# Kernel tuning notes

Hardware: AMD Instinct MI355X
Metric: run time of the kernel (lower is better)

Reference implementation:

```python
import jax, jax.numpy as jnp
import numpy as np

B, N, D = 8, 1024, 512
H = 8
DH = D // H
EPS_DIST = 1e-8
EPS_LN = 1e-5


def _layer_norm(x, gamma, beta):
    mu = jnp.mean(x, axis=-1, keepdims=True)
    var = jnp.mean((x - mu) ** 2, axis=-1, keepdims=True)
    return (x - mu) * jax.lax.rsqrt(var + EPS_LN) * gamma + beta


def setup_inputs() -> dict:
    key = jax.random.key(0)
    ks = jax.random.split(key, 6)
    scale = 1.0 / np.sqrt(D)
    inp = {
        "x": jax.random.normal(ks[0], (B, N, D), dtype=jnp.float32),
        "Wq": jax.random.normal(ks[1], (D, D), dtype=jnp.float32) * scale,
        "Wk": jax.random.normal(ks[2], (D, D), dtype=jnp.float32) * scale,
        "Wv": jax.random.normal(ks[3], (D, D), dtype=jnp.float32) * scale,
        "Wo": jax.random.normal(ks[4], (D, D), dtype=jnp.float32) * scale,
        "bq": jnp.zeros((D,), jnp.float32),
        "bk": jnp.zeros((D,), jnp.float32),
        "bv": jnp.zeros((D,), jnp.float32),
        "bo": jnp.zeros((D,), jnp.float32),
        "ln1_g": jnp.ones((D,), jnp.float32),
        "ln1_b": jnp.zeros((D,), jnp.float32),
        "ln2_g": jnp.ones((D,), jnp.float32),
        "ln2_b": jnp.zeros((D,), jnp.float32),
    }
    return inp


def reference(x, Wq, bq, Wk, bk, Wv, bv, Wo, bo, ln1_g, ln1_b, ln2_g, ln2_b):
    residual = x
    h = _layer_norm(x, ln1_g, ln1_b)  # pre-norm

    def heads(t):
        # [B,N,D] -> [B,H,N,DH]
        return t.reshape(B, N, H, DH).transpose(0, 2, 1, 3)

    q = heads(h @ Wq + bq)
    k = heads(h @ Wk + bk)
    v = heads(h @ Wv + bv)

    # Euclidean pairwise distance via ||q||^2 + ||k||^2 - 2 q.k expansion
    q_sq = jnp.sum(q * q, axis=-1)[..., :, None]      # [B,H,N,1]
    k_sq = jnp.sum(k * k, axis=-1)[..., None, :]      # [B,H,1,N]
    qk = jnp.einsum("bhnd,bhmd->bhnm", q, k)          # [B,H,N,N]
    d2 = jnp.maximum(q_sq + k_sq - 2.0 * qk, 0.0)
    dist = jnp.sqrt(d2 + EPS_DIST)

    # distance -> attention score: smaller distance = higher attention
    attn = jax.nn.softmax(-dist, axis=-1)             # [B,H,N,N]

    out = jnp.einsum("bhnm,bhmd->bhnd", attn, v)      # [B,H,N,DH]
    out = out.transpose(0, 2, 1, 3).reshape(B, N, D)
    out = out @ Wo + bo

    y = residual + out
    y = _layer_norm(y, ln2_g, ln2_b)
    return y
```

## Files before the change

kernel.cpp:

```cpp
#include <hip/hip_runtime.h>
#include <math.h>

typedef __attribute__((ext_vector_type(8))) short short8;
typedef __attribute__((ext_vector_type(4))) float f32x4;

constexpr int B  = 8;
constexpr int N  = 1024;
constexpr int D  = 512;
constexpr int H  = 8;
constexpr int DH = 64;
constexpr int M_ROWS = 8192;
constexpr float EPS_DIST = 1e-8f;
constexpr float EPS_LN   = 1e-5f;

__device__ inline unsigned short bfbits(float f) {
    union { float f; unsigned u; } v; v.f = f;
    unsigned r = v.u + 0x7fffu + ((v.u >> 16) & 1u);
    return (unsigned short)(r >> 16);
}
__device__ inline float bf2f(unsigned short s) {
    union { unsigned u; float f; } v; v.u = ((unsigned)s) << 16; return v.f;
}

__device__ inline void async_ld16(unsigned short* lds, const unsigned short* g) {
    __builtin_amdgcn_global_load_lds(
        (const __attribute__((address_space(1))) unsigned int*)(g),
        (__attribute__((address_space(3))) unsigned int*)(lds),
        16, 0, 0);
}

__device__ inline float block_sum256(float s, float* red) {
    for (int o = 32; o > 0; o >>= 1) s += __shfl_down(s, o, 64);
    int lane = threadIdx.x & 63, wid = threadIdx.x >> 6;
    if (lane == 0) red[wid] = s;
    __syncthreads();
    if (threadIdx.x == 0) red[4] = red[0] + red[1] + red[2] + red[3];
    __syncthreads();
    return red[4];
}

__global__ __launch_bounds__(256) void prep_kernel(const float* __restrict__ Wq,
                                                   const float* __restrict__ Wk,
                                                   const float* __restrict__ Wv,
                                                   const float* __restrict__ Wo,
                                                   unsigned short* __restrict__ WtAll,
                                                   const float* __restrict__ x,
                                                   const float* __restrict__ ln1_g,
                                                   const float* __restrict__ ln1_b,
                                                   unsigned short* __restrict__ h_bf) {
    __shared__ float red[8];
    const int bxg = blockIdx.x;
    if (bxg < 256) {
        int sub = bxg >> 6;
        const float* W = sub == 0 ? Wq : sub == 1 ? Wk : sub == 2 ? Wv : Wo;
        unsigned short* Wt = WtAll + (size_t)sub * 262144;
        int t = (bxg & 63) * 256 + threadIdx.x;
        int tn = t & 127, tk = t >> 7;
        int k = tk * 4, n = tn * 4;
        float4 r0 = *(const float4*)&W[(size_t)(k + 0) * 512 + n];
        float4 r1 = *(const float4*)&W[(size_t)(k + 1) * 512 + n];
        float4 r2 = *(const float4*)&W[(size_t)(k + 2) * 512 + n];
        float4 r3 = *(const float4*)&W[(size_t)(k + 3) * 512 + n];
        ushort4 c;
        c.x = bfbits(r0.x); c.y = bfbits(r1.x); c.z = bfbits(r2.x); c.w = bfbits(r3.x);
        *(ushort4*)&Wt[(size_t)(n + 0) * 512 + k] = c;
        c.x = bfbits(r0.y); c.y = bfbits(r1.y); c.z = bfbits(r2.y); c.w = bfbits(r3.y);
        *(ushort4*)&Wt[(size_t)(n + 1) * 512 + k] = c;
        c.x = bfbits(r0.z); c.y = bfbits(r1.z); c.z = bfbits(r2.z); c.w = bfbits(r3.z);
        *(ushort4*)&Wt[(size_t)(n + 2) * 512 + k] = c;
        c.x = bfbits(r0.w); c.y = bfbits(r1.w); c.z = bfbits(r2.w); c.w = bfbits(r3.w);
        *(ushort4*)&Wt[(size_t)(n + 3) * 512 + k] = c;
    } else {
        const int row = bxg - 256;
        const int t = threadIdx.x;
        const float* xr = x + (size_t)row * D;
        float v0 = xr[t], v1 = xr[t + 256];
        float mu = block_sum256(v0 + v1, red) * (1.0f / D);
        float d0 = v0 - mu, d1 = v1 - mu;
        float var = block_sum256(d0 * d0 + d1 * d1, red) * (1.0f / D);
        float rstd = rsqrtf(var + EPS_LN);
        h_bf[(size_t)row * D + t]       = bfbits(d0 * rstd * ln1_g[t] + ln1_b[t]);
        h_bf[(size_t)row * D + t + 256] = bfbits(d1 * rstd * ln1_g[t + 256] + ln1_b[t + 256]);
    }
}

__global__ __launch_bounds__(256) void ln2_kernel(const unsigned short* __restrict__ y0,
                                                  const float* __restrict__ res,
                                                  const float* __restrict__ gamma,
                                                  const float* __restrict__ beta,
                                                  float* __restrict__ out) {
    __shared__ float red[8];
    const int row = blockIdx.x;
    const int t = threadIdx.x;
    const unsigned short* xr = y0 + (size_t)row * D;
    const float* rr = res + (size_t)row * D;
    float v0 = bf2f(xr[t]) + rr[t];
    float v1 = bf2f(xr[t + 256]) + rr[t + 256];
    float mu = block_sum256(v0 + v1, red) * (1.0f / D);
    float d0 = v0 - mu, d1 = v1 - mu;
    float var = block_sum256(d0 * d0 + d1 * d1, red) * (1.0f / D);
    float rstd = rsqrtf(var + EPS_LN);
    out[(size_t)row * D + t]       = d0 * rstd * gamma[t] + beta[t];
    out[(size_t)row * D + t + 256] = d1 * rstd * gamma[t + 256] + beta[t + 256];
}

template <int MODE, int MT>
__global__ __launch_bounds__(256) void gemm128(const unsigned short* __restrict__ A,
                                               const unsigned short* __restrict__ Wt,
                                               const float* __restrict__ bias0,
                                               const float* __restrict__ bias1,
                                               const float* __restrict__ bias2,
                                               void* __restrict__ o0,
                                               unsigned short* __restrict__ Ko,
                                               unsigned short* __restrict__ Vo,
                                               float* __restrict__ sq0,
                                               float* __restrict__ sq1) {
    constexpr int RB = M_ROWS / MT;
    constexpr int NI = MT / 32;
    constexpr int ASZ = MT * 64, BSZ = 128 * 64;
    constexpr int SMSZ = (MODE == 1) ? ((ASZ + BSZ > 18432) ? ASZ + BSZ : 18432)
                                     : (ASZ + BSZ);
    __shared__ unsigned short smem[SMSZ];
    unsigned short* As = smem;
    unsigned short* Bs = smem + ASZ;

    const int id = blockIdx.x;
    const int by = id & (RB - 1), bx = id / RB;
    const int tid = threadIdx.x;
    const int lane = tid & 63, wv = tid >> 6;
    const int quad = lane >> 4, l15 = lane & 15;
    const int row0 = by * MT, col0 = bx * 128;
    const int wm = (wv & 1) * (MT / 2), wn = (wv >> 1) * 64;

    f32x4 acc[NI][4];
    #pragma unroll
    for (int i = 0; i < NI; ++i)
        #pragma unroll
        for (int j = 0; j < 4; ++j) acc[i][j] = (f32x4){0.f, 0.f, 0.f, 0.f};

    const unsigned short* Ag = A  + (size_t)row0 * 512;
    const unsigned short* Bg = Wt + (size_t)col0 * 512;

    for (int k0 = 0; k0 < 512; k0 += 64) {
        __syncthreads();
        #pragma unroll
        for (int c = 0; c < ASZ / 2048; ++c) {
            int fu = c * 2048 + tid * 8;
            int r = fu >> 6, ko = fu & 63;
            async_ld16(As + fu, Ag + (size_t)r * 512 + k0 + ko);
        }
        #pragma unroll
        for (int c = 0; c < BSZ / 2048; ++c) {
            int fu = c * 2048 + tid * 8;
            int r = fu >> 6, ko = fu & 63;
            async_ld16(Bs + fu, Bg + (size_t)r * 512 + k0 + ko);
        }
        __syncthreads();

        #pragma unroll
        for (int ks = 0; ks < 2; ++ks) {
            short8 af[NI], bf[4];
            #pragma unroll
            for (int i = 0; i < NI; ++i)
                af[i] = *(const short8*)&As[(wm + i * 16 + l15) * 64 + ks * 32 + quad * 8];
            #pragma unroll
            for (int j = 0; j < 4; ++j)
                bf[j] = *(const short8*)&Bs[(wn + j * 16 + l15) * 64 + ks * 32 + quad * 8];
            #pragma unroll
            for (int i = 0; i < NI; ++i)
                #pragma unroll
                for (int j = 0; j < 4; ++j)
                    acc[i][j] = __builtin_amdgcn_mfma_f32_16x16x32_bf16(af[i], bf[j], acc[i][j], 0, 0, 0);
        }
    }

    if (MODE == 0) {
        unsigned short* C = (unsigned short*)o0;
        #pragma unroll
        for (int i = 0; i < NI; ++i)
            #pragma unroll
            for (int j = 0; j < 4; ++j) {
                int col = col0 + wn + j * 16 + l15;
                float bv = bias0[col];
                #pragma unroll
                for (int r = 0; r < 4; ++r) {
                    int row = row0 + wm + i * 16 + quad * 4 + r;
                    C[(size_t)row * 512 + col] = bfbits(acc[i][j][r] + bv);
                }
            }
    } else {
        const int colg = col0 + wn;
        const int seg = colg >> 9;
        const int hh = (colg & 511) >> 6;
        const float* bias = seg == 0 ? bias0 : seg == 1 ? bias1 : bias2;

        if (seg < 2) {
            unsigned short* dst = seg == 0 ? (unsigned short*)o0 : Ko;
            float* sq = seg == 0 ? sq0 : sq1;
            #pragma unroll
            for (int i = 0; i < NI; ++i) {
                const int m0 = row0 + wm + i * 16 + quad * 4;
                float ss[4] = {0.f, 0.f, 0.f, 0.f};
                #pragma unroll
                for (int j = 0; j < 4; ++j) {
                    float bvj = bias[hh * 64 + j * 16 + l15];
                    #pragma unroll
                    for (int r = 0; r < 4; ++r) {
                        float v = acc[i][j][r] + bvj;
                        unsigned short ub = bfbits(v);
                        float vr = bf2f(ub);
                        ss[r] += vr * vr;
                        int m = m0 + r;
                        int b_ = m >> 10, n_ = m & 1023;
                        dst[((size_t)((b_ * 8 + hh) * 1024) + n_) * 64 + j * 16 + l15] = ub;
                    }
                }
                #pragma unroll
                for (int r = 0; r < 4; ++r) {
                    float s = ss[r];
                    s += __shfl_xor(s, 1, 64);
                    s += __shfl_xor(s, 2, 64);
                    s += __shfl_xor(s, 4, 64);
                    s += __shfl_xor(s, 8, 64);
                    if (l15 == 0) {
                        int m = m0 + r;
                        sq[(size_t)((m >> 10) * 8 + hh) * 1024 + (m & 1023)] = s;
                    }
                }
            }
        } else {
            __syncthreads();
            unsigned short* T = smem + wv * 4608;
            #pragma unroll
            for (int i = 0; i < NI; ++i)
                #pragma unroll
                for (int j = 0; j < 4; ++j) {
                    float bvj = bias[hh * 64 + j * 16 + l15];
                    ushort4 pk;
                    pk.x = bfbits(acc[i][j][0] + bvj);
                    pk.y = bfbits(acc[i][j][1] + bvj);
                    pk.z = bfbits(acc[i][j][2] + bvj);
                    pk.w = bfbits(acc[i][j][3] + bvj);
                    *(ushort4*)&T[(j * 16 + l15) * 72 + i * 16 + quad * 4] = pk;
                }
            const int b_ = (row0 + wm) >> 10;
            const int nbase = (row0 + wm) & 1023;
            unsigned short* Vg = Vo + ((size_t)((b_ * 8 + hh) * 64)) * 1024 + nbase;
            #pragma unroll
            for (int it = 0; it < 8; ++it) {
                int dl = it * 8 + (lane >> 3);
                int nl = (lane & 7) * 8;
                uint4 v = *(const uint4*)&T[dl * 72 + nl];
                *(uint4*)&Vg[(size_t)dl * 1024 + nl] = v;
            }
        }
    }
}

__global__ __launch_bounds__(512) void attn_kernel(const unsigned short* __restrict__ Q,
                                                   const unsigned short* __restrict__ K,
                                                   const unsigned short* __restrict__ Vt,
                                                   const float* __restrict__ qsq,
                                                   const float* __restrict__ ksq,
                                                   unsigned short* __restrict__ O) {
    __shared__ unsigned short Ks[2][64][72];
    __shared__ unsigned short Vs[2][64][72];
    __shared__ unsigned short Ps[8][16][72];
    __shared__ float ksq_s[2][64];

    const int id = blockIdx.x;
    const int bh = id & 63, qb = id >> 6;
    const int q0 = qb * 128;
    const int tid = threadIdx.x;
    const int lane = tid & 63, w = tid >> 6;
    const int quad = lane >> 4, l15 = lane & 15;
    const int b_ = bh >> 3, h_ = bh & 7;

    const unsigned short* Qb = Q  + (size_t)bh * N * DH;
    const unsigned short* Kb = K  + (size_t)bh * N * DH;
    const unsigned short* Vb = Vt + (size_t)bh * DH * N;

    short8 qf0, qf1;
    {
        const unsigned short* qp = Qb + (size_t)(q0 + w * 16 + l15) * 64 + quad * 8;
        qf0 = *(const short8*)qp;
        qf1 = *(const short8*)(qp + 32);
    }
    float qe[4];
    #pragma unroll
    for (int r = 0; r < 4; ++r)
        qe[r] = qsq[bh * N + q0 + w * 16 + quad * 4 + r] + EPS_DIST;

    f32x4 oacc[4];
    #pragma unroll
    for (int dt = 0; dt < 4; ++dt) oacc[dt] = (f32x4){0.f, 0.f, 0.f, 0.f};
    float dpart[4] = {};

    const int rr = tid >> 3, cc = (tid & 7) * 8;
    uint4 kreg, vreg;
    float ksreg = 0.f;

    kreg = *(const uint4*)(Kb + (size_t)rr * 64 + cc);
    vreg = *(const uint4*)(Vb + (size_t)rr * N + cc);
    if (tid < 64) ksreg = ksq[bh * N + tid];

    *(uint4*)&Ks[0][rr][cc] = kreg;
    *(uint4*)&Vs[0][rr][cc] = vreg;
    if (tid < 64) ksq_s[0][tid] = ksreg;
    __syncthreads();

    for (int kt = 0; kt < 16; ++kt) {
        const int cur = kt & 1;
        if (kt < 15) {
            kreg = *(const uint4*)(Kb + (size_t)((kt + 1) * 64 + rr) * 64 + cc);
            vreg = *(const uint4*)(Vb + (size_t)rr * N + (kt + 1) * 64 + cc);
            if (tid < 64) ksreg = ksq[bh * N + (kt + 1) * 64 + tid];
        }

        #pragma unroll
        for (int kb = 0; kb < 4; ++kb) {
            short8 kf0 = *(const short8*)&Ks[cur][kb * 16 + l15][quad * 8];
            short8 kf1 = *(const short8*)&Ks[cur][kb * 16 + l15][32 + quad * 8];
            float ks2 = ksq_s[cur][kb * 16 + l15];
            f32x4 sa = (f32x4){0.f, 0.f, 0.f, 0.f};
            sa = __builtin_amdgcn_mfma_f32_16x16x32_bf16(qf0, kf0, sa, 0, 0, 0);
            sa = __builtin_amdgcn_mfma_f32_16x16x32_bf16(qf1, kf1, sa, 0, 0, 0);
            #pragma unroll
            for (int r = 0; r < 4; ++r) {
                float d2 = fmaf(-2.0f, sa[r], qe[r] + ks2);
                d2 = fmaxf(d2, EPS_DIST);
                float p = __expf(-__builtin_amdgcn_sqrtf(d2));
                dpart[r] += p;
                union { float f; unsigned u; } pu; pu.f = p;
                Ps[w][quad * 4 + r][kb * 16 + l15] = (unsigned short)(pu.u >> 16);
            }
        }

        short8 vf[4][2];
        #pragma unroll
        for (int dt = 0; dt < 4; ++dt)
            #pragma unroll
            for (int kc = 0; kc < 2; ++kc)
                vf[dt][kc] = *(const short8*)&Vs[cur][dt * 16 + l15][kc * 32 + quad * 8];
        #pragma unroll
        for (int kc = 0; kc < 2; ++kc) {
            short8 pf = *(const short8*)&Ps[w][l15][kc * 32 + quad * 8];
            #pragma unroll
            for (int dt = 0; dt < 4; ++dt)
                oacc[dt] = __builtin_amdgcn_mfma_f32_16x16x32_bf16(pf, vf[dt][kc], oacc[dt], 0, 0, 0);
        }

        if (kt < 15) {
            *(uint4*)&Ks[cur ^ 1][rr][cc] = kreg;
            *(uint4*)&Vs[cur ^ 1][rr][cc] = vreg;
            if (tid < 64) ksq_s[cur ^ 1][tid] = ksreg;
        }
        __syncthreads();
    }

    float rinv[4];
    #pragma unroll
    for (int r = 0; r < 4; ++r) {
        float s = dpart[r];
        s += __shfl_xor(s, 1, 64);
        s += __shfl_xor(s, 2, 64);
        s += __shfl_xor(s, 4, 64);
        s += __shfl_xor(s, 8, 64);
        rinv[r] = 1.0f / s;
    }

    #pragma unroll
    for (int dt = 0; dt < 4; ++dt)
        #pragma unroll
        for (int r = 0; r < 4; ++r) {
            int n_ = q0 + w * 16 + quad * 4 + r;
            O[((size_t)(b_ * N + n_) * D) + h_ * DH + dt * 16 + l15] =
                bfbits(oacc[dt][r] * rinv[r]);
        }
}

extern "C" void kernel_launch(void* const* d_in, const int* in_sizes, int n_in,
                              void* d_out, int out_size, void* d_ws, size_t ws_size,
                              hipStream_t stream) {
    const float* x     = (const float*)d_in[0];
    const float* Wq    = (const float*)d_in[1];
    const float* Wk    = (const float*)d_in[2];
    const float* Wv    = (const float*)d_in[3];
    const float* Wo    = (const float*)d_in[4];
    const float* bq    = (const float*)d_in[5];
    const float* bk    = (const float*)d_in[6];
    const float* bv    = (const float*)d_in[7];
    const float* bo    = (const float*)d_in[8];
    const float* ln1_g = (const float*)d_in[9];
    const float* ln1_b = (const float*)d_in[10];
    const float* ln2_g = (const float*)d_in[11];
    const float* ln2_b = (const float*)d_in[12];
    float* out = (float*)d_out;

    unsigned short* WtAll = (unsigned short*)d_ws;
    unsigned short* h_bf  = WtAll + 4 * 262144;
    unsigned short* Qb    = h_bf + 4194304;
    unsigned short* Kb    = Qb + 4194304;
    unsigned short* Vtg   = Kb + 4194304;
    unsigned short* Ob    = Vtg + 4194304;
    unsigned short* Y0    = Ob + 4194304;
    float* qsq = (float*)(Y0 + 4194304);
    float* ksq = qsq + 65536;

    prep_kernel<<<256 + M_ROWS, 256, 0, stream>>>(Wq, Wk, Wv, Wo, WtAll,
                                                  x, ln1_g, ln1_b, h_bf);

    gemm128<1, 128><<<768, 256, 0, stream>>>(h_bf, WtAll, bq, bk, bv,
                                             Qb, Kb, Vtg, qsq, ksq);

    attn_kernel<<<512, 512, 0, stream>>>(Qb, Kb, Vtg, qsq, ksq, Ob);

    gemm128<0, 64><<<512, 256, 0, stream>>>(Ob, WtAll + 3 * 262144, bo,
                                            nullptr, nullptr, Y0,
                                            nullptr, nullptr, nullptr, nullptr);

    ln2_kernel<<<M_ROWS, 256, 0, stream>>>(Y0, x, ln2_g, ln2_b, out);
}
```

Before: 182.8 us.

## Fuse output projection with residual add and LayerNorm into one kernel

Replaces the separate output-projection GEMM and LN2 kernel with a single kernel. Each 512-thread block computes 32 full rows of the Wo projection, adds bias and residual, and applies LayerNorm in registers. This removes the bf16 Y0 round trip through global memory and one launch, and also keeps the pre-LN sum in fp32. In exchange the fused GEMM uses small 32-row tiles, reloads the full Wo panel per block, has no double buffering, and launches only 256 blocks. It also adds unroll 2 to the attention key-tile loop.

```diff
diff --git a/kernel.cpp b/kernel.cpp
--- a/kernel.cpp
+++ b/kernel.cpp
@@ -84,42 +84,21 @@
     }
 }
 
-__global__ __launch_bounds__(256) void ln2_kernel(const unsigned short* __restrict__ y0,
-                                                  const float* __restrict__ res,
-                                                  const float* __restrict__ gamma,
-                                                  const float* __restrict__ beta,
-                                                  float* __restrict__ out) {
-    __shared__ float red[8];
-    const int row = blockIdx.x;
-    const int t = threadIdx.x;
-    const unsigned short* xr = y0 + (size_t)row * D;
-    const float* rr = res + (size_t)row * D;
-    float v0 = bf2f(xr[t]) + rr[t];
-    float v1 = bf2f(xr[t + 256]) + rr[t + 256];
-    float mu = block_sum256(v0 + v1, red) * (1.0f / D);
-    float d0 = v0 - mu, d1 = v1 - mu;
-    float var = block_sum256(d0 * d0 + d1 * d1, red) * (1.0f / D);
-    float rstd = rsqrtf(var + EPS_LN);
-    out[(size_t)row * D + t]       = d0 * rstd * gamma[t] + beta[t];
-    out[(size_t)row * D + t + 256] = d1 * rstd * gamma[t + 256] + beta[t + 256];
-}
-
-template <int MODE, int MT>
-__global__ __launch_bounds__(256) void gemm128(const unsigned short* __restrict__ A,
-                                               const unsigned short* __restrict__ Wt,
-                                               const float* __restrict__ bias0,
-                                               const float* __restrict__ bias1,
-                                               const float* __restrict__ bias2,
-                                               void* __restrict__ o0,
-                                               unsigned short* __restrict__ Ko,
-                                               unsigned short* __restrict__ Vo,
-                                               float* __restrict__ sq0,
-                                               float* __restrict__ sq1) {
+template <int MT>
+__global__ __launch_bounds__(256) void gemm_qkv(const unsigned short* __restrict__ A,
+                                                const unsigned short* __restrict__ Wt,
+                                                const float* __restrict__ bias0,
+                                                const float* __restrict__ bias1,
+                                                const float* __restrict__ bias2,
+                                                unsigned short* __restrict__ Qo,
+                                                unsigned short* __restrict__ Ko,
+                                                unsigned short* __restrict__ Vo,
+                                                float* __restrict__ sq0,
+                                                float* __restrict__ sq1) {
     constexpr int RB = M_ROWS / MT;
     constexpr int NI = MT / 32;
     constexpr int ASZ = MT * 64, BSZ = 128 * 64;
-    constexpr int SMSZ = (MODE == 1) ? ((ASZ + BSZ > 18432) ? ASZ + BSZ : 18432)
-                                     : (ASZ + BSZ);
+    constexpr int SMSZ = (ASZ + BSZ > 18432) ? ASZ + BSZ : 18432;
     __shared__ unsigned short smem[SMSZ];
     unsigned short* As = smem;
     unsigned short* Bs = smem + ASZ;
@@ -174,85 +153,69 @@
         }
     }
 
-    if (MODE == 0) {
-        unsigned short* C = (unsigned short*)o0;
-        #pragma unroll
-        for (int i = 0; i < NI; ++i)
+    const int colg = col0 + wn;
+    const int seg = colg >> 9;
+    const int hh = (colg & 511) >> 6;
+    const float* bias = seg == 0 ? bias0 : seg == 1 ? bias1 : bias2;
+
+    if (seg < 2) {
+        unsigned short* dst = seg == 0 ? Qo : Ko;
+        float* sq = seg == 0 ? sq0 : sq1;
+        #pragma unroll
+        for (int i = 0; i < NI; ++i) {
+            const int m0 = row0 + wm + i * 16 + quad * 4;
+            float ss[4] = {0.f, 0.f, 0.f, 0.f};
             #pragma unroll
             for (int j = 0; j < 4; ++j) {
-                int col = col0 + wn + j * 16 + l15;
-                float bv = bias0[col];
+                float bvj = bias[hh * 64 + j * 16 + l15];
                 #pragma unroll
                 for (int r = 0; r < 4; ++r) {
-                    int row = row0 + wm + i * 16 + quad * 4 + r;
-                    C[(size_t)row * 512 + col] = bfbits(acc[i][j][r] + bv);
+                    float v = acc[i][j][r] + bvj;
+                    unsigned short ub = bfbits(v);
+                    float vr = bf2f(ub);
+                    ss[r] += vr * vr;
+                    int m = m0 + r;
+                    int b_ = m >> 10, n_ = m & 1023;
+                    dst[((size_t)((b_ * 8 + hh) * 1024) + n_) * 64 + j * 16 + l15] = ub;
                 }
             }
-    } else {
-        const int colg = col0 + wn;
-        const int seg = colg >> 9;
-        const int hh = (colg & 511) >> 6;
-        const float* bias = seg == 0 ? bias0 : seg == 1 ? bias1 : bias2;
-
-        if (seg < 2) {
-            unsigned short* dst = seg == 0 ? (unsigned short*)o0 : Ko;
-            float* sq = seg == 0 ? sq0 : sq1;
-            #pragma unroll
-            for (int i = 0; i < NI; ++i) {
-                const int m0 = row0 + wm + i * 16 + quad * 4;
-                float ss[4] = {0.f, 0.f, 0.f, 0.f};
-                #pragma unroll
-                for (int j = 0; j < 4; ++j) {
-                    float bvj = bias[hh * 64 + j * 16 + l15];
-                    #pragma unroll
-                    for (int r = 0; r < 4; ++r) {
-                        float v = acc[i][j][r] + bvj;
-                        unsigned short ub = bfbits(v);
-                        float vr = bf2f(ub);
-                        ss[r] += vr * vr;
-                        int m = m0 + r;
-                        int b_ = m >> 10, n_ = m & 1023;
-                        dst[((size_t)((b_ * 8 + hh) * 1024) + n_) * 64 + j * 16 + l15] = ub;
-                    }
-                }
-                #pragma unroll
-                for (int r = 0; r < 4; ++r) {
-                    float s = ss[r];
-                    s += __shfl_xor(s, 1, 64);
-                    s += __shfl_xor(s, 2, 64);
-                    s += __shfl_xor(s, 4, 64);
-                    s += __shfl_xor(s, 8, 64);
-                    if (l15 == 0) {
-                        int m = m0 + r;
-                        sq[(size_t)((m >> 10) * 8 + hh) * 1024 + (m & 1023)] = s;
-                    }
+            #pragma unroll
+            for (int r = 0; r < 4; ++r) {
+                float s = ss[r];
+                s += __shfl_xor(s, 1, 64);
+                s += __shfl_xor(s, 2, 64);
+                s += __shfl_xor(s, 4, 64);
+                s += __shfl_xor(s, 8, 64);
+                if (l15 == 0) {
+                    int m = m0 + r;
+                    sq[(size_t)((m >> 10) * 8 + hh) * 1024 + (m & 1023)] = s;
                 }
             }
-        } else {
-            __syncthreads();
-            unsigned short* T = smem + wv * 4608;
-            #pragma unroll
-            for (int i = 0; i < NI; ++i)
-                #pragma unroll
-                for (int j = 0; j < 4; ++j) {
-                    float bvj = bias[hh * 64 + j * 16 + l15];
-                    ushort4 pk;
-                    pk.x = bfbits(acc[i][j][0] + bvj);
-                    pk.y = bfbits(acc[i][j][1] + bvj);
-                    pk.z = bfbits(acc[i][j][2] + bvj);
-                    pk.w = bfbits(acc[i][j][3] + bvj);
-                    *(ushort4*)&T[(j * 16 + l15) * 72 + i * 16 + quad * 4] = pk;
-                }
-            const int b_ = (row0 + wm) >> 10;
-            const int nbase = (row0 + wm) & 1023;
-            unsigned short* Vg = Vo + ((size_t)((b_ * 8 + hh) * 64)) * 1024 + nbase;
-            #pragma unroll
-            for (int it = 0; it < 8; ++it) {
-                int dl = it * 8 + (lane >> 3);
-                int nl = (lane & 7) * 8;
-                uint4 v = *(const uint4*)&T[dl * 72 + nl];
-                *(uint4*)&Vg[(size_t)dl * 1024 + nl] = v;
+        }
+    } else {
+        __syncthreads();
+        unsigned short* T = smem + wv * 4608;
+        #pragma unroll
+        for (int i = 0; i < NI; ++i)
+            #pragma unroll
+            for (int j = 0; j < 4; ++j) {
+                float bvj = bias[hh * 64 + j * 16 + l15];
+                ushort4 pk;
+                pk.x = bfbits(acc[i][j][0] + bvj);
+                pk.y = bfbits(acc[i][j][1] + bvj);
+                pk.z = bfbits(acc[i][j][2] + bvj);
+                pk.w = bfbits(acc[i][j][3] + bvj);
+                *(ushort4*)&T[(j * 16 + l15) * 72 + i * 16 + quad * 4] = pk;
             }
+        const int b_ = (row0 + wm) >> 10;
+        const int nbase = (row0 + wm) & 1023;
+        unsigned short* Vg = Vo + ((size_t)((b_ * 8 + hh) * 64)) * 1024 + nbase;
+        #pragma unroll
+        for (int it = 0; it < 8; ++it) {
+            int dl = it * 8 + (lane >> 3);
+            int nl = (lane & 7) * 8;
+            uint4 v = *(const uint4*)&T[dl * 72 + nl];
+            *(uint4*)&Vg[(size_t)dl * 1024 + nl] = v;
         }
     }
 }
@@ -309,6 +272,7 @@
     if (tid < 64) ksq_s[0][tid] = ksreg;
     __syncthreads();
 
+    #pragma unroll 2
     for (int kt = 0; kt < 16; ++kt) {
         const int cur = kt & 1;
         if (kt < 15) {
@@ -377,6 +341,102 @@
             O[((size_t)(b_ * N + n_) * D) + h_ * DH + dt * 16 + l15] =
                 bfbits(oacc[dt][r] * rinv[r]);
         }
+}
+
+__global__ __launch_bounds__(512) void outln_kernel(const unsigned short* __restrict__ Ob,
+                                                    const unsigned short* __restrict__ WtO,
+                                                    const float* __restrict__ bo,
+                                                    const float* __restrict__ x,
+                                                    const float* __restrict__ gamma,
+                                                    const float* __restrict__ beta,
+                                                    float* __restrict__ out) {
+    __shared__ unsigned short As[32 * 40];
+    __shared__ unsigned short Bs[512 * 40];
+    __shared__ float redS[32][4];
+    __shared__ float redQ[32][4];
+
+    const int m0 = blockIdx.x * 32;
+    const int tid = threadIdx.x;
+    const int lane = tid & 63, w = tid >> 6;
+    const int quad = lane >> 4, l15 = lane & 15;
+    const int wr = (w & 1) * 16;
+    const int wc = (w >> 1) * 128;
+
+    f32x4 acc[8];
+    #pragma unroll
+    for (int j = 0; j < 8; ++j) acc[j] = (f32x4){0.f, 0.f, 0.f, 0.f};
+
+    const unsigned short* Ag = Ob + (size_t)m0 * 512;
+
+    for (int k0 = 0; k0 < 512; k0 += 32) {
+        __syncthreads();
+        #pragma unroll
+        for (int c = 0; c < 4; ++c)
+            *(uint4*)&Bs[tid * 40 + c * 8] = *(const uint4*)&WtO[(size_t)tid * 512 + k0 + c * 8];
+        if (tid < 128) {
+            int r = tid >> 2, c = tid & 3;
+            *(uint4*)&As[r * 40 + c * 8] = *(const uint4*)&Ag[(size_t)r * 512 + k0 + c * 8];
+        }
+        __syncthreads();
+
+        short8 af = *(const short8*)&As[(wr + l15) * 40 + quad * 8];
+        #pragma unroll
+        for (int j = 0; j < 8; ++j) {
+            short8 bf = *(const short8*)&Bs[(wc + j * 16 + l15) * 40 + quad * 8];
+            acc[j] = __builtin_amdgcn_mfma_f32_16x16x32_bf16(af, bf, acc[j], 0, 0, 0);
+        }
+    }
+
+    float bv[8], gv[8], bev[8];
+    #pragma unroll
+    for (int j = 0; j < 8; ++j) {
+        int col = wc + j * 16 + l15;
+        bv[j] = bo[col]; gv[j] = gamma[col]; bev[j] = beta[col];
+    }
+
+    float v[8][4];
+    float s1[4] = {0.f, 0.f, 0.f, 0.f}, s2[4] = {0.f, 0.f, 0.f, 0.f};
+    #pragma unroll
+    for (int r = 0; r < 4; ++r) {
+        int m = m0 + wr + quad * 4 + r;
+        #pragma unroll
+        for (int j = 0; j < 8; ++j) {
+            float t = acc[j][r] + bv[j] + x[(size_t)m * 512 + wc + j * 16 + l15];
+            v[j][r] = t;
+            s1[r] += t;
+            s2[r] += t * t;
+        }
+    }
+    #pragma unroll
+    for (int r = 0; r < 4; ++r) {
+        #pragma unroll
+        for (int o = 1; o < 16; o <<= 1) {
+            s1[r] += __shfl_xor(s1[r], o, 64);
+            s2[r] += __shfl_xor(s2[r], o, 64);
+        }
+    }
+    if (l15 == 0) {
+        #pragma unroll
+        for (int r = 0; r < 4; ++r) {
+            redS[wr + quad * 4 + r][w >> 1] = s1[r];
+            redQ[wr + quad * 4 + r][w >> 1] = s2[r];
+        }
+    }
+    __syncthreads();
+    #pragma unroll
+    for (int r = 0; r < 4; ++r) {
+        int lr = wr + quad * 4 + r;
+        float S = redS[lr][0] + redS[lr][1] + redS[lr][2] + redS[lr][3];
+        float Q2 = redQ[lr][0] + redQ[lr][1] + redQ[lr][2] + redQ[lr][3];
+        float mu = S * (1.0f / 512.0f);
+        float var = Q2 * (1.0f / 512.0f) - mu * mu;
+        float rstd = rsqrtf(var + EPS_LN);
+        int m = m0 + lr;
+        #pragma unroll
+        for (int j = 0; j < 8; ++j)
+            out[(size_t)m * 512 + wc + j * 16 + l15] =
+                (v[j][r] - mu) * rstd * gv[j] + bev[j];
+    }
 }
 
 extern "C" void kernel_launch(void* const* d_in, const int* in_sizes, int n_in,
@@ -403,21 +463,17 @@
     unsigned short* Kb    = Qb + 4194304;
     unsigned short* Vtg   = Kb + 4194304;
     unsigned short* Ob    = Vtg + 4194304;
-    unsigned short* Y0    = Ob + 4194304;
-    float* qsq = (float*)(Y0 + 4194304);
+    float* qsq = (float*)(Ob + 4194304);
     float* ksq = qsq + 65536;
 
     prep_kernel<<<256 + M_ROWS, 256, 0, stream>>>(Wq, Wk, Wv, Wo, WtAll,
                                                   x, ln1_g, ln1_b, h_bf);
 
-    gemm128<1, 128><<<768, 256, 0, stream>>>(h_bf, WtAll, bq, bk, bv,
-                                             Qb, Kb, Vtg, qsq, ksq);
+    gemm_qkv<128><<<768, 256, 0, stream>>>(h_bf, WtAll, bq, bk, bv,
+                                           Qb, Kb, Vtg, qsq, ksq);
 
     attn_kernel<<<512, 512, 0, stream>>>(Qb, Kb, Vtg, qsq, ksq, Ob);
 
-    gemm128<0, 64><<<512, 256, 0, stream>>>(Ob, WtAll + 3 * 262144, bo,
-                                            nullptr, nullptr, Y0,
-                                            nullptr, nullptr, nullptr, nullptr);
-
-    ln2_kernel<<<M_ROWS, 256, 0, stream>>>(Y0, x, ln2_g, ln2_b, out);
-}
+    outln_kernel<<<256, 512, 0, stream>>>(Ob, WtAll + 3 * 262144, bo,
+                                          x, ln2_g, ln2_b, out);
+}
```

Result: slower. 191.4 us (+4.7%).
